# Kernel tuning notes

Measured on AMD Instinct MI355X. Metric: run time of the kernel, lower is better.

## Reference

```python
import jax, jax.numpy as jnp
import numpy as np

E = 512   # embed_size
H = 8     # heads
D = E // H
WIN = 256 # window_size
N = 4     # batch
S = 2048  # seq len (query_len == key_len == value_len)


def setup_inputs() -> dict:
    key = jax.random.key(0)
    ks = jax.random.split(key, 8)
    s = 0.02
    inp = {
        "value": jax.random.normal(ks[0], (N, S, E), jnp.float32),
        "key":   jax.random.normal(ks[1], (N, S, E), jnp.float32),
        "query": jax.random.normal(ks[2], (N, S, E), jnp.float32),
        "mask":  jnp.ones((N, 1, 1, S), jnp.int32),
        # nn.Linear params: y = x @ W.T + b, W shape [out, in]
        "Wv": jax.random.normal(ks[3], (E, E), jnp.float32) * s,
        "bv": jnp.zeros((E,), jnp.float32),
        "Wk": jax.random.normal(ks[4], (E, E), jnp.float32) * s,
        "bk": jnp.zeros((E,), jnp.float32),
        "Wq": jax.random.normal(ks[5], (E, E), jnp.float32) * s,
        "bq": jnp.zeros((E,), jnp.float32),
        "Wo": jax.random.normal(ks[6], (E, E), jnp.float32) * s,
        "bo": jnp.zeros((E,), jnp.float32),
    }
    return inp


def reference(value, key, query, mask, Wv, bv, Wk, bk, Wq, bq, Wo, bo):
    n, q_len, _ = query.shape
    k_len = key.shape[1]
    w = min(WIN, k_len)  # window_size = min(self.window_size, key_len)

    v = (value @ Wv.T + bv).reshape(n, k_len, H, D)
    k = (key   @ Wk.T + bk).reshape(n, k_len, H, D)
    q = (query @ Wq.T + bq).reshape(n, q_len, H, D)

    # Full QK scores; banded window selected below. Position j is inside the
    # window of query i iff  i - w//2 <= j <= i + w//2 (matches the torch
    # per-i slice [max(0,i-w//2), min(k_len, i+w//2+1)) ).
    scores = jnp.einsum('nqhd,nkhd->nhqk', q, k)  # [N,H,Q,K]
    ii = jnp.arange(q_len)[:, None]
    jj = jnp.arange(k_len)[None, :]
    in_win = (jj >= ii - w // 2) & (jj <= ii + w // 2)  # [Q,K]

    # Inside window: scores, masked to -inf where mask == 0.
    # Outside window: entries stay 0 (the torch code zero-inits attention).
    neg_inf = jnp.float32(-jnp.inf)
    banded = jnp.where(mask != 0, scores, neg_inf)          # broadcast [N,1,1,K]
    att_logits = jnp.where(in_win[None, None], banded, 0.0)  # [N,H,Q,K]

    att_logits = att_logits / jnp.sqrt(jnp.float32(E))  # scale by sqrt(embed_size)
    attention = jax.nn.softmax(att_logits, axis=3)

    out = jnp.einsum('nhqk,nkhd->nqhd', attention, v).reshape(n, q_len, E)
    out = out @ Wo.T + bo
    return (out, attention)
```

## Files before the change

kernel.cpp:

```cpp
#include <hip/hip_runtime.h>


typedef unsigned short u16;
typedef __bf16 bf16x8 __attribute__((ext_vector_type(8)));
typedef float  f32x4  __attribute__((ext_vector_type(4)));
typedef u16    u16x8  __attribute__((ext_vector_type(8)));

#define GLOAD_LDS(gsrc, ldst)                                                  \
    __builtin_amdgcn_global_load_lds(                                          \
        (const __attribute__((address_space(1))) void*)(gsrc),                 \
        (__attribute__((address_space(3))) void*)(ldst), 16, 0, 0)

__device__ __forceinline__ u16 f2bf(float f) {
    union { float f; unsigned u; } x; x.f = f;
    unsigned u = x.u;
    u += 0x7fffu + ((u >> 16) & 1u);
    return (u16)(u >> 16);
}
__device__ __forceinline__ int swzc(int c, int r) {
    return (c < 32) ? (c ^ (r & 7)) : c;
}

struct CvtWArgs {
    const float* src[4];
    u16*         dst[4];
};

__global__ __launch_bounds__(256) void cvt_w(CvtWArgs a) {
    int t = blockIdx.x >> 8, blk = blockIdx.x & 255;
    int i = (blk * 256 + threadIdx.x) * 4;
    float4 v = *(const float4*)(a.src[t] + i);
    ushort4 o;
    o.x = f2bf(v.x); o.y = f2bf(v.y); o.z = f2bf(v.z); o.w = f2bf(v.w);
    *(ushort4*)(a.dst[t] + i) = o;
}

__global__ __launch_bounds__(256) void gemm_qkv(
    const float* __restrict__ A0, const float* __restrict__ A1, const float* __restrict__ A2,
    const u16* __restrict__ B,
    const float* __restrict__ b0, const float* __restrict__ b1, const float* __restrict__ b2,
    u16* __restrict__ o0, u16* __restrict__ o1, u16* __restrict__ o2,
    float* __restrict__ sumv)
{
    __shared__ __attribute__((aligned(16))) u16 As[128 * 64];
    __shared__ __attribute__((aligned(16))) u16 Bs[128 * 64];

    const int tid  = threadIdx.x;
    const int lane = tid & 63;
    const int w    = tid >> 6;
    const int bm   = blockIdx.x, bn = blockIdx.y;
    const int wm   = w >> 1, wn = w & 1;

    const int t = bn >> 2;
    const float* A = (t == 0) ? A0 : (t == 1) ? A1 : A2;
    const float* Ag = A + (size_t)bm * 128 * 512;
    const u16* Bg = B + (size_t)bn * 128 * 512;

    f32x4 acc[4][4];
#pragma unroll
    for (int m = 0; m < 4; ++m)
#pragma unroll
        for (int n = 0; n < 4; ++n) acc[m][n] = 0;

    const int swc = ((lane & 7) ^ (lane >> 3)) * 8;
    const int arow = tid >> 1, ahalf = tid & 1;
    const float* asrc = Ag + (size_t)arow * 512 + ahalf * 32;

    for (int k0 = 0; k0 < 512; k0 += 64) {
        float4 fv[8];
#pragma unroll
        for (int i = 0; i < 8; ++i) fv[i] = *(const float4*)(asrc + k0 + i * 4);
#pragma unroll
        for (int c4 = 0; c4 < 4; ++c4) {
            bf16x8 pk;
#pragma unroll
            for (int e = 0; e < 8; ++e) {
                float f = ((const float*)&fv[c4 * 2])[e];
                pk[e] = (__bf16)f;
            }
            int ch = ahalf * 4 + c4;
            *(bf16x8*)(As + arow * 64 + ((ch ^ (arow & 7)) * 8)) = pk;
        }
#pragma unroll
        for (int i = 0; i < 4; ++i) {
            int g = i * 4 + w;
            GLOAD_LDS(Bg + (size_t)(g * 8 + (lane >> 3)) * 512 + k0 + swc, Bs + g * 512);
        }
        __syncthreads();

#pragma unroll
        for (int s = 0; s < 2; ++s) {
            bf16x8 af[4], bf[4];
            int c = s * 4 + (lane >> 4);
#pragma unroll
            for (int m = 0; m < 4; ++m) {
                int r = wm * 64 + m * 16 + (lane & 15);
                af[m] = *(const bf16x8*)(As + r * 64 + ((c ^ (r & 7)) * 8));
                int r2 = wn * 64 + m * 16 + (lane & 15);
                bf[m] = *(const bf16x8*)(Bs + r2 * 64 + ((c ^ (r2 & 7)) * 8));
            }
#pragma unroll
            for (int m = 0; m < 4; ++m)
#pragma unroll
                for (int n = 0; n < 4; ++n)
                    acc[m][n] = __builtin_amdgcn_mfma_f32_16x16x32_bf16(af[m], bf[n], acc[m][n], 0, 0, 0);
        }
        __syncthreads();
    }

    const float* bias = (t == 0) ? b0 : (t == 1) ? b1 : b2;
    u16* ob = (t == 0) ? o0 : (t == 1) ? o1 : o2;
    const int clbase = (bn & 3) * 128;

#pragma unroll
    for (int m = 0; m < 4; ++m) {
#pragma unroll
        for (int n = 0; n < 4; ++n) {
            int cl = clbase + wn * 64 + n * 16 + (lane & 15);
            float bb = bias[cl];
#pragma unroll
            for (int reg = 0; reg < 4; ++reg) {
                int row = bm * 128 + wm * 64 + m * 16 + (lane >> 4) * 4 + reg;
                ob[(size_t)row * 512 + cl] = f2bf(acc[m][n][reg] + bb);
            }
        }
    }

    if (t == 2) {
        int nb = bm >> 4;
#pragma unroll
        for (int n = 0; n < 4; ++n) {
            float s = 0.f;
#pragma unroll
            for (int m = 0; m < 4; ++m)
#pragma unroll
                for (int reg = 0; reg < 4; ++reg) s += acc[m][n][reg];
            s += __shfl_xor(s, 16, 64);
            s += __shfl_xor(s, 32, 64);
            if (lane < 16) {
                int cl = clbase + wn * 64 + n * 16 + lane;
                atomicAdd(sumv + nb * 512 + cl, s);
            }
        }
    }
}

__global__ __launch_bounds__(256) void gemm_o(
    const u16* __restrict__ A, const u16* __restrict__ B,
    const float* __restrict__ bias, float* __restrict__ fo)
{
    __shared__ __attribute__((aligned(16))) u16 As[128 * 64];
    __shared__ __attribute__((aligned(16))) u16 Bs[64 * 64];

    const int tid  = threadIdx.x;
    const int lane = tid & 63;
    const int w    = tid >> 6;
    const int bm   = blockIdx.x, bn = blockIdx.y;
    const int wm   = w >> 1, wn = w & 1;

    const u16* Ag = A + (size_t)bm * 128 * 512;
    const u16* Bg = B + (size_t)bn * 64 * 512;

    f32x4 acc[4][2];
#pragma unroll
    for (int m = 0; m < 4; ++m) { acc[m][0] = 0; acc[m][1] = 0; }

    const int swc = ((lane & 7) ^ (lane >> 3)) * 8;

    for (int k0 = 0; k0 < 512; k0 += 64) {
#pragma unroll
        for (int i = 0; i < 4; ++i) {
            int g = i * 4 + w;
            GLOAD_LDS(Ag + (size_t)(g * 8 + (lane >> 3)) * 512 + k0 + swc, As + g * 512);
        }
#pragma unroll
        for (int i = 0; i < 2; ++i) {
            int g = i * 4 + w;
            GLOAD_LDS(Bg + (size_t)(g * 8 + (lane >> 3)) * 512 + k0 + swc, Bs + g * 512);
        }
        __syncthreads();

#pragma unroll
        for (int s = 0; s < 2; ++s) {
            bf16x8 af[4], bf[2];
            int c = s * 4 + (lane >> 4);
#pragma unroll
            for (int m = 0; m < 4; ++m) {
                int r = wm * 64 + m * 16 + (lane & 15);
                af[m] = *(const bf16x8*)(As + r * 64 + ((c ^ (r & 7)) * 8));
            }
#pragma unroll
            for (int n = 0; n < 2; ++n) {
                int r2 = wn * 32 + n * 16 + (lane & 15);
                bf[n] = *(const bf16x8*)(Bs + r2 * 64 + ((c ^ (r2 & 7)) * 8));
            }
#pragma unroll
            for (int m = 0; m < 4; ++m)
#pragma unroll
                for (int n = 0; n < 2; ++n)
                    acc[m][n] = __builtin_amdgcn_mfma_f32_16x16x32_bf16(af[m], bf[n], acc[m][n], 0, 0, 0);
        }
        __syncthreads();
    }

#pragma unroll
    for (int m = 0; m < 4; ++m) {
#pragma unroll
        for (int n = 0; n < 2; ++n) {
            int cl = bn * 64 + wn * 32 + n * 16 + (lane & 15);
            float bb = bias[cl];
#pragma unroll
            for (int reg = 0; reg < 4; ++reg) {
                int row = bm * 128 + wm * 64 + m * 16 + (lane >> 4) * 4 + reg;
                fo[(size_t)row * 512 + cl] = acc[m][n][reg] + bb;
            }
        }
    }
}

__global__ __launch_bounds__(256) void attn_kernel(
    const u16* __restrict__ qb, const u16* __restrict__ kb,
    const u16* __restrict__ vb, const int* __restrict__ mask,
    const float* __restrict__ sumv, float* __restrict__ att,
    u16* __restrict__ oh) {
    __shared__ __attribute__((aligned(16))) char lds[78848];
    u16*   Qs      = (u16*)lds;
    float* stat_m  = (float*)lds;
    float* stat_rd = (float*)(lds + 128);
    float* stat_c  = (float*)(lds + 256);
    float* red     = (float*)(lds + 384);
    float* red2    = (float*)(lds + 640);
    u16*   Ks      = (u16*)(lds + 4096);
    u16*   Ab      = Ks;
    u16*   Vt      = (u16*)(lds + 4096 + 36864);

    const int tid  = threadIdx.x;
    const int lane = tid & 63;
    const int w    = tid >> 6;
    const int bid0 = blockIdx.x;
    const int bid  = (bid0 & 7) * 256 + (bid0 >> 3);
    const int tile = bid & 63;
    const int h    = (bid >> 6) & 7;
    const int n    = bid >> 9;
    const int i0   = tile * 32;
    const int jlo  = max(0, i0 - 128);
    const float scale = 0.04419417382415922f;

    const size_t base_nh = (size_t)n * 2048 * 512 + h * 64;
    const int lr = lane >> 3;
    const int swg = ((lane & 7) ^ lr) * 8;

    GLOAD_LDS(qb + base_nh + (size_t)(i0 + w * 8 + lr) * 512 + swg, Qs + w * 512);
    for (int p = 0; p < 9; ++p) {
        int g = p * 4 + w;
        int j = min(jlo + g * 8 + lr, 2047);
        GLOAD_LDS(kb + base_nh + (size_t)j * 512 + swg, Ks + g * 512);
    }
    for (int p = 0; p < 9; ++p) {
        int idx = p * 256 + tid;
        int jj = idx >> 3, ch = idx & 7;
        int j = jlo + jj;
        u16x8 tmp = {0, 0, 0, 0, 0, 0, 0, 0};
        if (j < 2048) tmp = *(const u16x8*)(vb + base_nh + (size_t)j * 512 + ch * 8);
        int jc = jj >> 3, jr = jj & 7;
        int pjc = (jc < 32) ? (jc ^ ch) : jc;
#pragma unroll
        for (int r = 0; r < 8; ++r)
            Vt[(ch * 8 + r) * 296 + pjc * 8 + jr] = tmp[r];
    }
    __syncthreads();

    const int rbase = (w & 1) * 16;
    const int cbase = (w >> 1) * 144;
    f32x4 acc[9];
#pragma unroll
    for (int f = 0; f < 9; ++f) acc[f] = 0;

    bf16x8 aq[2];
    {
        int r = rbase + (lane & 15);
#pragma unroll
        for (int ks = 0; ks < 2; ++ks) {
            int kc = ks * 4 + (lane >> 4);
            aq[ks] = *(const bf16x8*)(Qs + r * 64 + ((kc ^ (r & 7)) * 8));
        }
    }
#pragma unroll
    for (int f = 0; f < 9; ++f) {
        int jj = cbase + f * 16 + (lane & 15);
#pragma unroll
        for (int ks = 0; ks < 2; ++ks) {
            int kc = ks * 4 + (lane >> 4);
            bf16x8 bk_ = *(const bf16x8*)(Ks + jj * 64 + ((kc ^ (jj & 7)) * 8));
            acc[f] = __builtin_amdgcn_mfma_f32_16x16x32_bf16(aq[ks], bk_, acc[f], 0, 0, 0);
        }
    }
    __syncthreads();

    const int rowg = (lane >> 4) * 4;
    f32x4 lv[9];
    float mx[4] = {-__builtin_inff(), -__builtin_inff(), -__builtin_inff(), -__builtin_inff()};
#pragma unroll
    for (int f = 0; f < 9; ++f) {
        int jj = cbase + f * 16 + (lane & 15);
        int j = jlo + jj;
        int mk = (j < 2048) ? mask[n * 2048 + j] : 0;
#pragma unroll
        for (int reg = 0; reg < 4; ++reg) {
            int i = i0 + rbase + rowg + reg;
            bool inw = (j >= i - 128) && (j <= i + 128) && (j < 2048);
            float val = (inw && mk != 0) ? acc[f][reg] * scale : -__builtin_inff();
            lv[f][reg] = val;
            mx[reg] = fmaxf(mx[reg], val);
        }
    }
#pragma unroll
    for (int mskk = 1; mskk < 16; mskk <<= 1)
#pragma unroll
        for (int reg = 0; reg < 4; ++reg)
            mx[reg] = fmaxf(mx[reg], __shfl_xor(mx[reg], mskk, 64));
    if ((lane & 15) == 0) {
#pragma unroll
        for (int reg = 0; reg < 4; ++reg) red[w * 16 + rowg + reg] = mx[reg];
    }
    __syncthreads();
    if (tid < 32) {
        int r = tid;
        int wa = (r < 16) ? 0 : 1, rr = r & 15;
        stat_m[r] = fmaxf(fmaxf(red[wa * 16 + rr], red[(wa + 2) * 16 + rr]), 0.0f);
    }
    __syncthreads();

    float m4[4];
#pragma unroll
    for (int reg = 0; reg < 4; ++reg) m4[reg] = stat_m[rbase + rowg + reg];
    float sm[4] = {0, 0, 0, 0};
#pragma unroll
    for (int f = 0; f < 9; ++f)
#pragma unroll
        for (int reg = 0; reg < 4; ++reg)
            sm[reg] += __expf(lv[f][reg] - m4[reg]);
#pragma unroll
    for (int mskk = 1; mskk < 16; mskk <<= 1)
#pragma unroll
        for (int reg = 0; reg < 4; ++reg)
            sm[reg] += __shfl_xor(sm[reg], mskk, 64);
    if ((lane & 15) == 0) {
#pragma unroll
        for (int reg = 0; reg < 4; ++reg) red2[w * 16 + rowg + reg] = sm[reg];
    }
    __syncthreads();
    if (tid < 32) {
        int r = tid, gi = i0 + r;
        int wa = (r < 16) ? 0 : 1, rr = r & 15;
        float s = red2[wa * 16 + rr] + red2[(wa + 2) * 16 + rr];
        int lo = max(0, gi - 128), hi = min(2048, gi + 129);
        float em = __expf(-stat_m[r]);
        float denom = s + (float)(2048 - (hi - lo)) * em;
        float rd = 1.0f / denom;
        stat_rd[r] = rd;
        stat_c[r] = em * rd;
    }
    __syncthreads();

    float rd4[4], c4[4];
#pragma unroll
    for (int reg = 0; reg < 4; ++reg) {
        rd4[reg] = stat_rd[rbase + rowg + reg];
        c4[reg] = stat_c[rbase + rowg + reg];
    }
#pragma unroll
    for (int f = 0; f < 9; ++f) {
        int jj = cbase + f * 16 + (lane & 15);
        int j = jlo + jj;
        int jc = jj >> 3;
#pragma unroll
        for (int reg = 0; reg < 4; ++reg) {
            int it = rbase + rowg + reg;
            int i = i0 + it;
            bool inw = (j >= i - 128) && (j <= i + 128) && (j < 2048);
            float e = __expf(lv[f][reg] - m4[reg]);
            float a = inw ? e * rd4[reg] : c4[reg];
            if (j < 2048)
                att[((size_t)(n * 8 + h) * 2048 + i) * 2048 + j] = a;
            float ab = inw ? (a - c4[reg]) : 0.0f;
            ((u16*)((char*)Ab + it * 576 + (swzc(jc, it) << 4)))[jj & 7] = f2bf(ab);
        }
    }
    __syncthreads();

    const int rb2 = (w & 1) * 16;
    const int db  = (w >> 1) * 32;
    f32x4 po[2];
    po[0] = 0; po[1] = 0;
#pragma unroll
    for (int ks = 0; ks < 9; ++ks) {
        int kc = ks * 4 + (lane >> 4);
        int it = rb2 + (lane & 15);
        bf16x8 af = *(const bf16x8*)((char*)Ab + it * 576 + (swzc(kc, it) << 4));
#pragma unroll
        for (int f = 0; f < 2; ++f) {
            int d = db + f * 16 + (lane & 15);
            int phys = (kc < 32) ? (kc ^ (d >> 3)) : kc;
            bf16x8 bv_ = *(const bf16x8*)(Vt + d * 296 + phys * 8);
            po[f] = __builtin_amdgcn_mfma_f32_16x16x32_bf16(af, bv_, po[f], 0, 0, 0);
        }
    }
    {
        const float* svp = sumv + (size_t)n * 512 + h * 64;
#pragma unroll
        for (int f = 0; f < 2; ++f) {
            int d = db + f * 16 + (lane & 15);
            float sv = svp[d];
#pragma unroll
            for (int reg = 0; reg < 4; ++reg) {
                int it = rb2 + rowg + reg;
                float val = po[f][reg] + stat_c[it] * sv;
                oh[base_nh + (size_t)(i0 + it) * 512 + d] = f2bf(val);
            }
        }
    }

    {
        int jend = min(2048, jlo + 288);
        int j4lo = jlo >> 2, j4end = jend >> 2;
        size_t rowbase = ((size_t)(n * 8 + h) * 2048 + i0) * 2048;
        for (int idx = tid; idx < 32 * 512; idx += 256) {
            int r = idx >> 9, j4 = idx & 511;
            if (j4 >= j4lo && j4 < j4end) continue;
            float c = stat_c[r];
            *(float4*)(att + rowbase + (size_t)r * 2048 + j4 * 4) = make_float4(c, c, c, c);
        }
    }
}

extern "C" void kernel_launch(void* const* d_in, const int* in_sizes, int n_in,
                              void* d_out, int out_size, void* d_ws, size_t ws_size,
                              hipStream_t stream) {
    const float* value = (const float*)d_in[0];
    const float* key_  = (const float*)d_in[1];
    const float* query = (const float*)d_in[2];
    const int*   mask  = (const int*)d_in[3];
    const float* Wv = (const float*)d_in[4];
    const float* bv = (const float*)d_in[5];
    const float* Wk = (const float*)d_in[6];
    const float* bk = (const float*)d_in[7];
    const float* Wq = (const float*)d_in[8];
    const float* bq = (const float*)d_in[9];
    const float* Wo = (const float*)d_in[10];
    const float* bo = (const float*)d_in[11];

    char* ws = (char*)d_ws;
    size_t off = 0;
    auto carve = [&](size_t bytes) -> char* {
        char* p = ws + off;
        off += (bytes + 255) & ~(size_t)255;
        return p;
    };
    const size_t XB = (size_t)8192 * 512 * 2;
    const size_t WB = (size_t)512 * 512 * 2;
    u16* wqkv = (u16*)carve(3 * WB);
    u16* wob  = (u16*)carve(WB);
    u16* qb   = (u16*)carve(XB);
    u16* kb   = (u16*)carve(XB);
    u16* vb2  = (u16*)carve(XB);
    u16* ohb  = (u16*)carve(XB);
    float* sumv = (float*)carve(2048 * sizeof(float));

    hipMemsetAsync(sumv, 0, 2048 * sizeof(float), stream);

    CvtWArgs ca;
    ca.src[0] = Wq; ca.dst[0] = wqkv;
    ca.src[1] = Wk; ca.dst[1] = wqkv + (size_t)512 * 512;
    ca.src[2] = Wv; ca.dst[2] = wqkv + (size_t)1024 * 512;
    ca.src[3] = Wo; ca.dst[3] = wob;

    cvt_w<<<dim3(1024), 256, 0, stream>>>(ca);
    gemm_qkv<<<dim3(64, 12), 256, 0, stream>>>(
        query, key_, value, wqkv, bq, bk, bv, qb, kb, vb2, sumv);

    float* att = (float*)d_out + (size_t)4 * 2048 * 512;
    attn_kernel<<<dim3(2048), 256, 0, stream>>>(qb, kb, vb2, mask, sumv, att, ohb);
    gemm_o<<<dim3(64, 8), 256, 0, stream>>>(ohb, wob, bo, (float*)d_out);
}
```

Before: 663.4 us.

## Stage attention probabilities in fp32 LDS and write full rows with coalesced nontemporal stores

Softmax probabilities (minus the out-of-window constant) are now kept in an fp32 LDS buffer rather than a swizzled bf16 buffer. The per-lane scattered global stores of the in-window attention entries are removed. The final fill loop now writes every row of the attention matrix as float4 nontemporal stores, adding the LDS value back inside the window, so all output writes are coalesced and bypass cache. The cost is a larger LDS footprint, bf16 conversion moved into the MFMA operand load, and possible bank conflicts from the unswizzled fp32 layout.

Result: faster. 643.6 us (-3.0%).

```diff
diff --git a/kernel.cpp b/kernel.cpp
--- a/kernel.cpp
+++ b/kernel.cpp
@@ -16,9 +16,6 @@
     unsigned u = x.u;
     u += 0x7fffu + ((u >> 16) & 1u);
     return (u16)(u >> 16);
-}
-__device__ __forceinline__ int swzc(int c, int r) {
-    return (c < 32) ? (c ^ (r & 7)) : c;
 }
 
 struct CvtWArgs {
@@ -223,7 +220,7 @@
     const u16* __restrict__ vb, const int* __restrict__ mask,
     const float* __restrict__ sumv, float* __restrict__ att,
     u16* __restrict__ oh) {
-    __shared__ __attribute__((aligned(16))) char lds[78848];
+    __shared__ __attribute__((aligned(16))) char lds[79616];
     u16*   Qs      = (u16*)lds;
     float* stat_m  = (float*)lds;
     float* stat_rd = (float*)(lds + 128);
@@ -231,8 +228,8 @@
     float* red     = (float*)(lds + 384);
     float* red2    = (float*)(lds + 640);
     u16*   Ks      = (u16*)(lds + 4096);
-    u16*   Ab      = Ks;
-    u16*   Vt      = (u16*)(lds + 4096 + 36864);
+    float* Ab32    = (float*)(lds + 4096);
+    u16*   Vt      = (u16*)(lds + 4096 + 37632);
 
     const int tid  = threadIdx.x;
     const int lane = tid & 63;
@@ -373,18 +370,13 @@
     for (int f = 0; f < 9; ++f) {
         int jj = cbase + f * 16 + (lane & 15);
         int j = jlo + jj;
-        int jc = jj >> 3;
 #pragma unroll
         for (int reg = 0; reg < 4; ++reg) {
             int it = rbase + rowg + reg;
             int i = i0 + it;
             bool inw = (j >= i - 128) && (j <= i + 128) && (j < 2048);
             float e = __expf(lv[f][reg] - m4[reg]);
-            float a = inw ? e * rd4[reg] : c4[reg];
-            if (j < 2048)
-                att[((size_t)(n * 8 + h) * 2048 + i) * 2048 + j] = a;
-            float ab = inw ? (a - c4[reg]) : 0.0f;
-            ((u16*)((char*)Ab + it * 576 + (swzc(jc, it) << 4)))[jj & 7] = f2bf(ab);
+            Ab32[it * 292 + jj] = inw ? (e * rd4[reg] - c4[reg]) : 0.0f;
         }
     }
     __syncthreads();
@@ -397,7 +389,14 @@
     for (int ks = 0; ks < 9; ++ks) {
         int kc = ks * 4 + (lane >> 4);
         int it = rb2 + (lane & 15);
-        bf16x8 af = *(const bf16x8*)((char*)Ab + it * 576 + (swzc(kc, it) << 4));
+        const float* ap = Ab32 + it * 292 + kc * 8;
+        float4 alo = *(const float4*)(ap);
+        float4 ahi = *(const float4*)(ap + 4);
+        bf16x8 af;
+        af[0] = (__bf16)alo.x; af[1] = (__bf16)alo.y;
+        af[2] = (__bf16)alo.z; af[3] = (__bf16)alo.w;
+        af[4] = (__bf16)ahi.x; af[5] = (__bf16)ahi.y;
+        af[6] = (__bf16)ahi.z; af[7] = (__bf16)ahi.w;
 #pragma unroll
         for (int f = 0; f < 2; ++f) {
             int d = db + f * 16 + (lane & 15);
@@ -423,13 +422,17 @@
 
     {
         int jend = min(2048, jlo + 288);
-        int j4lo = jlo >> 2, j4end = jend >> 2;
         size_t rowbase = ((size_t)(n * 8 + h) * 2048 + i0) * 2048;
         for (int idx = tid; idx < 32 * 512; idx += 256) {
             int r = idx >> 9, j4 = idx & 511;
-            if (j4 >= j4lo && j4 < j4end) continue;
+            int j = j4 * 4;
             float c = stat_c[r];
-            *(float4*)(att + rowbase + (size_t)r * 2048 + j4 * 4) = make_float4(c, c, c, c);
+            f32x4 v = {c, c, c, c};
+            if (j >= jlo && j < jend) {
+                const float* ap = Ab32 + r * 292 + (j - jlo);
+                v[0] += ap[0]; v[1] += ap[1]; v[2] += ap[2]; v[3] += ap[3];
+            }
+            __builtin_nontemporal_store(v, (f32x4*)(att + rowbase + (size_t)r * 2048 + j));
         }
     }
 }
@@ -467,7 +470,7 @@
     u16* ohb  = (u16*)carve(XB);
     float* sumv = (float*)carve(2048 * sizeof(float));
 
-    hipMemsetAsync(sumv, 0, 2048 * sizeof(float), stream);
+    (void)hipMemsetAsync(sumv, 0, 2048 * sizeof(float), stream);
 
     CvtWArgs ca;
     ca.src[0] = Wq; ca.dst[0] = wqkv;
```
